# Kernel tuning notes

Measured on AMD Instinct MI355X. Metric: run time of the kernel, lower is better.

Reference implementation:

```python
import jax, jax.numpy as jnp
import numpy as np
from jax import lax

B, T, I, H, O = 512, 4096, 1, 16, 1  # batch, seq_len, input_size, hidden_size, output_size


def setup_inputs() -> dict:
    key = jax.random.key(0)
    ks = jax.random.split(key, 7)
    s = 1.0 / np.sqrt(H)  # PyTorch uniform(-1/sqrt(H), 1/sqrt(H)) init scale
    u = lambda k, shape: jax.random.uniform(k, shape, jnp.float32, -s, s)
    return {
        "x": jax.random.normal(ks[0], (B, T, I), jnp.float32),
        "W_ih": u(ks[1], (4 * H, I)),
        "W_hh": u(ks[2], (4 * H, H)),
        "b_ih": u(ks[3], (4 * H,)),
        "b_hh": u(ks[4], (4 * H,)),
        "W_fc": u(ks[5], (O, H)),
        "b_fc": u(ks[6], (O,)),
    }


def reference(x, W_ih, W_hh, b_ih, b_hh, W_fc, b_fc):
    # Single-layer LSTM, batch_first, dropout forced to 0 when n_layers==1.
    # Precompute input projection for all timesteps (hoisted out of the scan).
    xW = jnp.einsum('bti,gi->btg', x, W_ih) + b_ih + b_hh  # [B, T, 4H]
    xW_t = jnp.swapaxes(xW, 0, 1)  # [T, B, 4H]

    def step(carry, xt):
        h, c = carry
        gates = xt + h @ W_hh.T  # [B, 4H]; PyTorch gate order: i, f, g, o
        i, f, g, o = jnp.split(gates, 4, axis=-1)
        i = jax.nn.sigmoid(i)
        f = jax.nn.sigmoid(f)
        g = jnp.tanh(g)
        o = jax.nn.sigmoid(o)
        c = f * c + i * g
        h = o * jnp.tanh(c)
        return (h, c), h

    h0 = jnp.zeros((B, H), x.dtype)
    c0 = jnp.zeros((B, H), x.dtype)
    _, hs = lax.scan(step, (h0, c0), xW_t)  # hs: [T, B, H]
    hs = jnp.swapaxes(hs, 0, 1)  # [B, T, H]
    out = hs @ W_fc.T + b_fc  # [B, T, O]
    return out
```

## Files before the change

### kernel.cpp

```cpp
#include <hip/hip_runtime.h>
#include <hip/hip_bf16.h>


constexpr int NB = 512;
constexpr int NT = 4096;

typedef _Float16 half2_t __attribute__((ext_vector_type(2)));
typedef __fp16   fp16v2  __attribute__((ext_vector_type(2)));

template<int CTRL>
__device__ __forceinline__ float qbcast(float x) {
  return __int_as_float(__builtin_amdgcn_mov_dpp(__float_as_int(x), CTRL, 0xF, 0xF, true));
}
__device__ __forceinline__ float dpp_shl4(float x) {
  return __int_as_float(__builtin_amdgcn_mov_dpp(__float_as_int(x), 0x104, 0xF, 0xF, true));
}
__device__ __forceinline__ int rdlane_i(int x, int lane) {
  return __builtin_amdgcn_readlane(x, lane);
}
__device__ __forceinline__ float rdlane(float x, int lane) {
  return __int_as_float(__builtin_amdgcn_readlane(__float_as_int(x), lane));
}
__device__ __forceinline__ float vexp2(float x) {
  float r; asm("v_exp_f32 %0, %1" : "=v"(r) : "v"(x)); return r;
}
__device__ __forceinline__ float vrcp(float x) {
  float r; asm("v_rcp_f32 %0, %1" : "=v"(r) : "v"(x)); return r;
}
__device__ __forceinline__ half2_t h2_from_i(int x) {
  union { int i; half2_t h; } u; u.i = x; return u.h;
}
__device__ __forceinline__ int pack_f16(float lo, float hi) {
  union { fp16v2 v; int i; } u; u.v = __builtin_amdgcn_cvt_pkrtz(lo, hi); return u.i;
}

__global__ __launch_bounds__(64, 1) void lstm_fused(
    const float* __restrict__ x,
    const float* __restrict__ W_ih,
    const float* __restrict__ W_hh,
    const float* __restrict__ b_ih,
    const float* __restrict__ b_hh,
    const float* __restrict__ W_fc,
    const float* __restrict__ b_fc,
    float* __restrict__ out)
{
  __shared__ float tile[64 * 65];
  const int b = blockIdx.x;
  const int l = threadIdx.x;
  const int j = l >> 2;
  const int k = l & 3;
  const int r = k * 16 + j;

  constexpr float LOG2E = 1.4426950408889634f;
  constexpr float K2    = -2.0f * LOG2E;
  const float sc = (k == 2) ? K2 : -LOG2E;

  half2_t w2[8];
  #pragma unroll
  for (int q = 0; q < 8; ++q) {
    w2[q][0] = (_Float16)(W_hh[r * 16 + 2 * q + 0] * sc);
    w2[q][1] = (_Float16)(W_hh[r * 16 + 2 * q + 1] * sc);
  }
  const float wx    = W_ih[r] * sc;
  const float wb    = (b_ih[r] + b_hh[r]) * sc;
  const float act_m = (k == 2) ? (2.0f * K2) : 1.0f;
  const float act_a = (k == 2) ? (-K2)       : 0.0f;
  const float wfc   = W_fc[j] * 0.25f;
  const float bfc   = b_fc[0];

  const float* xb = x + (size_t)b * NT;
  float*       ob = out + (size_t)b * NT;

  float cs = 0.0f;
  int sp[8];
  #pragma unroll
  for (int q = 0; q < 8; ++q) sp[q] = 0;

  float xcur = xb[l];

  for (int blk = 0; blk < NT / 64; ++blk) {
    float xnext = 0.0f;
    if (blk + 1 < NT / 64) xnext = xb[(blk + 1) * 64 + l];

    #pragma unroll 16
    for (int tt = 0; tt < 64; ++tt) {
      const float sx    = rdlane(xcur, tt);
      const float xinit = fmaf(wx, sx, wb);
      float a0 = __builtin_amdgcn_fdot2(w2[0], h2_from_i(sp[0]), xinit, false);
      float a1 = __builtin_amdgcn_fdot2(w2[1], h2_from_i(sp[1]), 0.0f,  false);
      #pragma unroll
      for (int q = 2; q < 8; q += 2) {
        a0 = __builtin_amdgcn_fdot2(w2[q + 0], h2_from_i(sp[q + 0]), a0, false);
        a1 = __builtin_amdgcn_fdot2(w2[q + 1], h2_from_i(sp[q + 1]), a1, false);
      }
      const float z   = a0 + a1;
      const float e1  = vexp2(z);
      const float r1  = vrcp(1.0f + e1);
      const float act = fmaf(r1, act_m, act_a);
      const float ii  = qbcast<0x00>(act);
      const float ff  = qbcast<0x55>(act);
      const float ggs = qbcast<0xAA>(act);
      const float oo  = qbcast<0xFF>(act);
      const float oo2 = oo + oo;
      cs = fmaf(ff, cs, ii * ggs);
      const float e2 = vexp2(cs);
      const float r2 = vrcp(1.0f + e2);
      const float h  = fmaf(oo2, r2, -oo);
      tile[tt * 65 + l] = h * wfc;
      const float hn = dpp_shl4(h);
      const int   hi = pack_f16(h, hn);
      #pragma unroll
      for (int q = 0; q < 8; ++q) sp[q] = rdlane_i(hi, 8 * q);
    }

    float s0 = bfc, s1 = 0.0f, s2 = 0.0f, s3 = 0.0f;
    #pragma unroll
    for (int i2 = 0; i2 < 64; i2 += 4) {
      s0 += tile[l * 65 + i2 + 0];
      s1 += tile[l * 65 + i2 + 1];
      s2 += tile[l * 65 + i2 + 2];
      s3 += tile[l * 65 + i2 + 3];
    }
    ob[blk * 64 + l] = (s0 + s1) + (s2 + s3);
    xcur = xnext;
  }
}

extern "C" void kernel_launch(void* const* d_in, const int* in_sizes, int n_in,
                              void* d_out, int out_size, void* d_ws, size_t ws_size,
                              hipStream_t stream) {
  const float* x    = (const float*)d_in[0];
  const float* W_ih = (const float*)d_in[1];
  const float* W_hh = (const float*)d_in[2];
  const float* b_ih = (const float*)d_in[3];
  const float* b_hh = (const float*)d_in[4];
  const float* W_fc = (const float*)d_in[5];
  const float* b_fc = (const float*)d_in[6];
  float* out = (float*)d_out;
  (void)in_sizes; (void)n_in; (void)out_size; (void)d_ws; (void)ws_size;
  lstm_fused<<<NB, 64, 0, stream>>>(x, W_ih, W_hh, b_ih, b_hh, W_fc, b_fc, out);
}
```

Baseline: 396.0 us.

## Pack eight batch wavefronts per block and shrink per-wave output tile

Launches 64 blocks of 8 wavefronts (one batch row per wave) instead of 512 single-wave blocks, and cuts the per-wave LDS tile from 64x65 to 16x65 by flushing the output projection every 16 timesteps. The reduction now uses four lanes per row plus DPP quad permutes. The aim is to fit more waves per CU with less shared memory and better placement, at the cost of more frequent flush phases and fewer blocks to spread across CUs.

Measured after the change: 669.2 us. +69.0%, slower.

```diff
diff --git a/kernel.cpp b/kernel.cpp
--- a/kernel.cpp
+++ b/kernel.cpp
@@ -2,14 +2,19 @@
 #include <hip/hip_bf16.h>
 
 
-constexpr int NB = 512;
-constexpr int NT = 4096;
+constexpr int NB  = 512;
+constexpr int NT  = 4096;
+constexpr int WPB = 8;
 
 typedef _Float16 half2_t __attribute__((ext_vector_type(2)));
 typedef __fp16   fp16v2  __attribute__((ext_vector_type(2)));
 
 template<int CTRL>
 __device__ __forceinline__ float qbcast(float x) {
+  return __int_as_float(__builtin_amdgcn_mov_dpp(__float_as_int(x), CTRL, 0xF, 0xF, true));
+}
+template<int CTRL>
+__device__ __forceinline__ float qperm(float x) {
   return __int_as_float(__builtin_amdgcn_mov_dpp(__float_as_int(x), CTRL, 0xF, 0xF, true));
 }
 __device__ __forceinline__ float dpp_shl4(float x) {
@@ -34,7 +39,7 @@
   union { fp16v2 v; int i; } u; u.v = __builtin_amdgcn_cvt_pkrtz(lo, hi); return u.i;
 }
 
-__global__ __launch_bounds__(64, 1) void lstm_fused(
+__global__ __launch_bounds__(512, 2) void lstm_fused(
     const float* __restrict__ x,
     const float* __restrict__ W_ih,
     const float* __restrict__ W_hh,
@@ -44,12 +49,14 @@
     const float* __restrict__ b_fc,
     float* __restrict__ out)
 {
-  __shared__ float tile[64 * 65];
-  const int b = blockIdx.x;
-  const int l = threadIdx.x;
-  const int j = l >> 2;
-  const int k = l & 3;
-  const int r = k * 16 + j;
+  __shared__ float tile[WPB][16 * 65];
+  const int wid = threadIdx.x >> 6;
+  const int l   = threadIdx.x & 63;
+  const int b   = blockIdx.x * WPB + wid;
+  const int j   = l >> 2;
+  const int k   = l & 3;
+  const int r   = k * 16 + j;
+  float* mytile = &tile[wid][0];
 
   constexpr float LOG2E = 1.4426950408889634f;
   constexpr float K2    = -2.0f * LOG2E;
@@ -82,46 +89,53 @@
     float xnext = 0.0f;
     if (blk + 1 < NT / 64) xnext = xb[(blk + 1) * 64 + l];
 
-    #pragma unroll 16
-    for (int tt = 0; tt < 64; ++tt) {
-      const float sx    = rdlane(xcur, tt);
-      const float xinit = fmaf(wx, sx, wb);
-      float a0 = __builtin_amdgcn_fdot2(w2[0], h2_from_i(sp[0]), xinit, false);
-      float a1 = __builtin_amdgcn_fdot2(w2[1], h2_from_i(sp[1]), 0.0f,  false);
+    #pragma unroll 1
+    for (int sub = 0; sub < 4; ++sub) {
+      const int tbase = sub * 16;
+
       #pragma unroll
-      for (int q = 2; q < 8; q += 2) {
-        a0 = __builtin_amdgcn_fdot2(w2[q + 0], h2_from_i(sp[q + 0]), a0, false);
-        a1 = __builtin_amdgcn_fdot2(w2[q + 1], h2_from_i(sp[q + 1]), a1, false);
+      for (int tt = 0; tt < 16; ++tt) {
+        const float sx    = rdlane(xcur, tbase + tt);
+        const float xinit = fmaf(wx, sx, wb);
+        float a0 = __builtin_amdgcn_fdot2(w2[0], h2_from_i(sp[0]), xinit, false);
+        float a1 = __builtin_amdgcn_fdot2(w2[1], h2_from_i(sp[1]), 0.0f,  false);
+        #pragma unroll
+        for (int q = 2; q < 8; q += 2) {
+          a0 = __builtin_amdgcn_fdot2(w2[q + 0], h2_from_i(sp[q + 0]), a0, false);
+          a1 = __builtin_amdgcn_fdot2(w2[q + 1], h2_from_i(sp[q + 1]), a1, false);
+        }
+        const float z   = a0 + a1;
+        const float e1  = vexp2(z);
+        const float r1  = vrcp(1.0f + e1);
+        const float act = fmaf(r1, act_m, act_a);
+        const float ii  = qbcast<0x00>(act);
+        const float ff  = qbcast<0x55>(act);
+        const float ggs = qbcast<0xAA>(act);
+        const float oo  = qbcast<0xFF>(act);
+        const float oo2 = oo + oo;
+        cs = fmaf(ff, cs, ii * ggs);
+        const float e2 = vexp2(cs);
+        const float r2 = vrcp(1.0f + e2);
+        const float h  = fmaf(oo2, r2, -oo);
+        mytile[tt * 65 + l] = h * wfc;
+        const float hn = dpp_shl4(h);
+        const int   hi = pack_f16(h, hn);
+        #pragma unroll
+        for (int q = 0; q < 8; ++q) sp[q] = rdlane_i(hi, 8 * q);
       }
-      const float z   = a0 + a1;
-      const float e1  = vexp2(z);
-      const float r1  = vrcp(1.0f + e1);
-      const float act = fmaf(r1, act_m, act_a);
-      const float ii  = qbcast<0x00>(act);
-      const float ff  = qbcast<0x55>(act);
-      const float ggs = qbcast<0xAA>(act);
-      const float oo  = qbcast<0xFF>(act);
-      const float oo2 = oo + oo;
-      cs = fmaf(ff, cs, ii * ggs);
-      const float e2 = vexp2(cs);
-      const float r2 = vrcp(1.0f + e2);
-      const float h  = fmaf(oo2, r2, -oo);
-      tile[tt * 65 + l] = h * wfc;
-      const float hn = dpp_shl4(h);
-      const int   hi = pack_f16(h, hn);
-      #pragma unroll
-      for (int q = 0; q < 8; ++q) sp[q] = rdlane_i(hi, 8 * q);
+
+      {
+        const int row = l >> 2;
+        const int q4  = l & 3;
+        float s = 0.0f;
+        #pragma unroll
+        for (int i2 = 0; i2 < 16; ++i2)
+          s += mytile[row * 65 + q4 * 16 + i2];
+        s += qperm<0xB1>(s);
+        s += qperm<0x4E>(s);
+        if (q4 == 0) ob[blk * 64 + tbase + row] = s + bfc;
+      }
     }
-
-    float s0 = bfc, s1 = 0.0f, s2 = 0.0f, s3 = 0.0f;
-    #pragma unroll
-    for (int i2 = 0; i2 < 64; i2 += 4) {
-      s0 += tile[l * 65 + i2 + 0];
-      s1 += tile[l * 65 + i2 + 1];
-      s2 += tile[l * 65 + i2 + 2];
-      s3 += tile[l * 65 + i2 + 3];
-    }
-    ob[blk * 64 + l] = (s0 + s1) + (s2 + s3);
     xcur = xnext;
   }
 }
@@ -138,5 +152,5 @@
   const float* b_fc = (const float*)d_in[6];
   float* out = (float*)d_out;
   (void)in_sizes; (void)n_in; (void)out_size; (void)d_ws; (void)ws_size;
-  lstm_fused<<<NB, 64, 0, stream>>>(x, W_ih, W_hh, b_ih, b_hh, W_fc, b_fc, out);
+  lstm_fused<<<NB / WPB, WPB * 64, 0, stream>>>(x, W_ih, W_hh, b_ih, b_hh, W_fc, b_fc, out);
 }
```
